# Performance work log

Hardware: AMD Instinct MI355X
Metric: run time of the kernel (lower is better)

The kernel has to match this reference:

```python
import jax, jax.numpy as jnp
import numpy as np

COMMITMENT_COST = 0.25

def setup_inputs() -> dict:
    key = jax.random.key(0)
    k1, k2 = jax.random.split(key)
    B, d_latent = 8192, 512
    ncb, K, d_sub = 2, 8192, 256
    z = jax.random.normal(k1, (B, d_latent), dtype=jnp.float32)
    # original inits uniform(-1/K, 1/K)
    embedding = jax.random.uniform(k2, (ncb, K, d_sub), dtype=jnp.float32,
                                   minval=-1.0 / K, maxval=1.0 / K)
    return {"z": z, "embedding": embedding}


def reference(z, embedding):
    B, d_latent = z.shape
    ncb, K, d_sub = embedding.shape
    z_split = z.reshape(B, ncb, d_sub)

    # squared euclidean distances [B, ncb, K] via ||z||^2 - 2 z.e + ||e||^2
    z_sq = jnp.sum(z_split * z_split, axis=-1)          # [B, ncb]
    e_sq = jnp.sum(embedding * embedding, axis=-1)      # [ncb, K]
    cross = jnp.einsum('bnd,nkd->bnk', z_split, embedding)  # [B, ncb, K]
    distances = z_sq[:, :, None] - 2.0 * cross + e_sq[None, :, :]

    indices = jnp.argmin(distances, axis=-1)            # [B, ncb] int

    # gather quantized vectors: q[b, n] = embedding[n, indices[b, n]]
    cb_ids = jnp.arange(ncb)[None, :]                   # [1, ncb]
    z_q = embedding[cb_ids, indices]                    # [B, ncb, d_sub]

    commitment_loss = COMMITMENT_COST * jnp.mean(
        (z_split - jax.lax.stop_gradient(z_q)) ** 2)
    codebook_loss = jnp.array(0.0, dtype=z.dtype)       # use_ema=True, eval mode

    # straight-through estimator
    z_q_st = z_split + jax.lax.stop_gradient(z_q - z_split)
    quantized = z_q_st.reshape(B, d_latent)

    # perplexity: mean one-hot usage over batch, averaged across codebooks
    counts = jnp.zeros((ncb, K), dtype=z.dtype).at[cb_ids, indices].add(1.0)
    avg_probs = jnp.mean(counts / B, axis=0)            # [K]
    perplexity = jnp.exp(-jnp.sum(avg_probs * jnp.log(avg_probs + 1e-10)))

    return quantized, indices, commitment_loss, codebook_loss, perplexity
```

## Files before the change

### kernel.cpp

```cpp
#include <hip/hip_runtime.h>
#include <hip/hip_fp16.h>


#define KCODES 8192
#define DSUB   256
#define BROWS  8192
#define NROWS  16384
#define NWIN   512

#define QUANT_N  (BROWS * 512)
#define IDX_OFF  QUANT_N
#define LOSS_OFF (QUANT_N + NROWS)

#define WS_ESQ     0
#define WS_ZSQ     65536
#define WS_ZSCL    131072
#define WS_WINNER  262144
#define WS_ZQ      1048576
#define WS_EQ8     5242880
#define WS_TM      9437184

#define EPS 2.5e-4f
#define SE_INV (8192.0f * 127.0f)
#define SE (1.0f / SE_INV)


typedef __attribute__((ext_vector_type(4)))  int int4v;
typedef __attribute__((ext_vector_type(16))) int int16v;

__device__ inline void gl2lds16(const void* g, void* l) {
  __builtin_amdgcn_global_load_lds(
      (const __attribute__((address_space(1))) void*)g,
      (__attribute__((address_space(3))) void*)l, 16, 0, 0);
}

__device__ inline int imax2(int a, int b) { return a > b ? a : b; }

__global__ __launch_bounds__(256)
void prep_kernel(const float* __restrict__ z, const float* __restrict__ e,
                 float* __restrict__ e_sq, float* __restrict__ z_sq,
                 float* __restrict__ z_scl,
                 char* __restrict__ zq, char* __restrict__ eq8,
                 unsigned long long* __restrict__ winner) {
  __shared__ char xfer[4][8192];
  int t = blockIdx.x * 256 + threadIdx.x;
  if (t < 16384) winner[t] = ~0ull;

  const int w = threadIdx.x >> 6, lane = threadIdx.x & 63;
  const int gi = blockIdx.x * 4 + w;
  const int q = lane >> 4, c = lane & 15;
  const bool is_e = gi < 512;
  const int n = (gi >> 8) & 1, g = gi & 255;

  char* dst = (is_e ? eq8 : zq) + (size_t)n * 2097152 + (size_t)g * 8192;

  #pragma unroll 2
  for (int i = 0; i < 8; ++i) {
    const int rr = i * 4 + q;
    const float* src;
    if (is_e) src = e + ((size_t)(n * KCODES + g * 32 + rr)) * DSUB;
    else      src = z + ((size_t)(g * 32 + rr)) * 512 + n * 256;

    float4 f[4];
    float ssq = 0.f, mx = 0.f;
    #pragma unroll
    for (int j = 0; j < 4; ++j) {
      f[j] = *(const float4*)(src + 4 * c + 64 * j);
      ssq += f[j].x * f[j].x + f[j].y * f[j].y + f[j].z * f[j].z + f[j].w * f[j].w;
      mx = fmaxf(mx, fmaxf(fmaxf(fabsf(f[j].x), fabsf(f[j].y)),
                           fmaxf(fabsf(f[j].z), fabsf(f[j].w))));
    }
    #pragma unroll
    for (int off = 8; off; off >>= 1) {
      ssq += __shfl_xor(ssq, off, 16);
      mx = fmaxf(mx, __shfl_xor(mx, off, 16));
    }
    float inv, s = 0.f;
    if (is_e) {
      inv = SE_INV;
    } else {
      s = fmaxf(mx, 1e-20f) * (1.0f / 127.0f);
      inv = 1.0f / s;
    }
    if (c == 0) {
      if (is_e) {
        e_sq[n * KCODES + g * 32 + rr] = ssq;
      } else {
        z_sq[(g * 32 + rr) * 2 + n] = ssq;
        z_scl[n * KCODES + g * 32 + rr] = s;
      }
    }
    #pragma unroll
    for (int j = 0; j < 4; ++j) {
      unsigned acc = 0;
      int q0 = __float2int_rn(fminf(fmaxf(f[j].x * inv, -127.f), 127.f));
      int q1 = __float2int_rn(fminf(fmaxf(f[j].y * inv, -127.f), 127.f));
      int q2 = __float2int_rn(fminf(fmaxf(f[j].z * inv, -127.f), 127.f));
      int q3 = __float2int_rn(fminf(fmaxf(f[j].w * inv, -127.f), 127.f));
      acc = ((unsigned)(q0 & 255)) | ((unsigned)(q1 & 255) << 8)
          | ((unsigned)(q2 & 255) << 16) | ((unsigned)(q3 & 255) << 24);
      const int k = 4 * c + 64 * j;
      const int off = (k >> 5) * 1024 + ((k >> 4) & 1) * 512 + rr * 16 + (k & 15);
      *(unsigned*)&xfer[w][off] = acc;
    }
  }
  __syncthreads();
  #pragma unroll
  for (int it = 0; it < 8; ++it)
    *(uint4*)(dst + it * 1024 + lane * 16) = *(const uint4*)&xfer[w][it * 1024 + lane * 16];
}

__global__ __launch_bounds__(256, 2)
void passA_kernel(const char* __restrict__ zq, const char* __restrict__ eq8,
                  const float* __restrict__ z_scl,
                  unsigned* __restrict__ tm32, int rowoff) {
  __shared__ char Bs[2][8192];

  const int n    = blockIdx.z;
  const int tid  = threadIdx.x;
  const int w    = tid >> 6, lane = tid & 63;
  const int l5   = lane >> 5, c32 = lane & 31;
  const int cb   = blockIdx.x * 512 + w * 128;
  const int rg   = rowoff + blockIdx.y * 256;

  const char* en = eq8 + (size_t)n * 2097152;
  const char* zn = zq + (size_t)n * 2097152;
  const float* zscl = z_scl + n * KCODES;
  unsigned* tmn = tm32 + (size_t)n * (4096 * NWIN);

  const int lo8 = l5 * 512 + c32 * 16;

  int4v areg[8][4];
  #pragma unroll
  for (int k0 = 0; k0 < 8; ++k0)
    #pragma unroll
    for (int mi = 0; mi < 4; ++mi)
      areg[k0][mi] = *(const int4v*)(en + (size_t)((cb >> 5) + mi) * 8192
                                     + k0 * 1024 + lo8);

  const char* zg = zn + (size_t)(rg >> 5) * 8192;
  #pragma unroll
  for (int j = 0; j < 2; ++j)
    gl2lds16(zg + w * 2048 + j * 1024 + lane * 16, &Bs[0][w * 2048 + j * 1024]);

  for (int nt = 0; nt < 8; ++nt) {
    __syncthreads();
    if (nt < 7) {
      const char* zs = zg + (nt + 1) * 8192;
      char* ld = &Bs[(nt + 1) & 1][0];
      #pragma unroll
      for (int j = 0; j < 2; ++j)
        gl2lds16(zs + w * 2048 + j * 1024 + lane * 16, ld + w * 2048 + j * 1024);
    }
    const char* bsrc = &Bs[nt & 1][0];
    const int rowbase = rg + nt * 32;

    const float sv = 2.0f * SE * zscl[rowbase + c32];
    const int thr_i = (int)fminf(EPS / sv, 1.0e9f) + 1;

    int16v acc[4];
    #pragma unroll
    for (int mi = 0; mi < 4; ++mi)
      #pragma unroll
      for (int i = 0; i < 16; ++i) acc[mi][i] = 0;

    #pragma unroll
    for (int k0 = 0; k0 < 8; ++k0) {
      int4v b0 = *(const int4v*)&bsrc[k0 * 1024 + lo8];
      __builtin_amdgcn_s_setprio(1);
      acc[0] = __builtin_amdgcn_mfma_i32_32x32x32_i8(areg[k0][0], b0, acc[0], 0, 0, 0);
      acc[1] = __builtin_amdgcn_mfma_i32_32x32x32_i8(areg[k0][1], b0, acc[1], 0, 0, 0);
      acc[2] = __builtin_amdgcn_mfma_i32_32x32x32_i8(areg[k0][2], b0, acc[2], 0, 0, 0);
      acc[3] = __builtin_amdgcn_mfma_i32_32x32x32_i8(areg[k0][3], b0, acc[3], 0, 0, 0);
      __builtin_amdgcn_s_setprio(0);
    }

    unsigned wd[8];
    #pragma unroll
    for (int mi = 0; mi < 4; ++mi) {
      int mx0 = imax2(imax2(imax2(acc[mi][0], acc[mi][1]), imax2(acc[mi][2], acc[mi][3])),
                      imax2(imax2(acc[mi][4], acc[mi][5]), imax2(acc[mi][6], acc[mi][7])));
      int mx1 = imax2(imax2(imax2(acc[mi][8], acc[mi][9]), imax2(acc[mi][10], acc[mi][11])),
                      imax2(imax2(acc[mi][12], acc[mi][13]), imax2(acc[mi][14], acc[mi][15])));
      mx0 = imax2(mx0, __shfl_xor(mx0, 32, 64));
      mx1 = imax2(mx1, __shfl_xor(mx1, 32, 64));
      unsigned a0 = 0, b0m = 0;
      #pragma unroll
      for (int r = 0; r < 8; ++r) {
        const int bp = (r & 3) + 8 * (r >> 2);
        a0  |= (unsigned)(mx0 - acc[mi][r] <= thr_i) << bp;
        b0m |= (unsigned)(mx1 - acc[mi][r + 8] <= thr_i) << bp;
      }
      a0 <<= 4 * l5;
      b0m <<= 4 * l5;
      a0  |= (unsigned)__shfl_xor((int)a0, 32, 64);
      b0m |= (unsigned)__shfl_xor((int)b0m, 32, 64);
      const float m0f = -sv * (float)mx0;
      const float m1f = -sv * (float)mx1;
      wd[mi * 2]     = (unsigned)__half_as_ushort(__float2half(m0f)) | (a0 << 16);
      wd[mi * 2 + 1] = (unsigned)__half_as_ushort(__float2half(m1f)) | (b0m << 16);
    }
    if (l5 == 0) {
      int zr = rowbase + c32;
      unsigned* dst = &tmn[(size_t)(zr - rowoff) * NWIN + (cb >> 4)];
      uint4 o0; o0.x = wd[0]; o0.y = wd[1]; o0.z = wd[2]; o0.w = wd[3];
      uint4 o1; o1.x = wd[4]; o1.y = wd[5]; o1.z = wd[6]; o1.w = wd[7];
      *(uint4*)dst = o0;
      *(uint4*)(dst + 4) = o1;
    }
  }
}

__global__ __launch_bounds__(256)
void passB12_kernel(const unsigned* __restrict__ tm32, const float* __restrict__ z,
                    const float* __restrict__ emb, const float* __restrict__ e_sq,
                    const float* __restrict__ z_sq,
                    unsigned long long* __restrict__ winner, int rzoff) {
  __shared__ unsigned buf[4][128];

  const int w = threadIdx.x >> 6, lane = threadIdx.x & 63;
  const int gw = blockIdx.x * 4 + w;
  const int r0 = rzoff + gw * 2;
  const int boff = rzoff >> 1;

  unsigned cnt = 0;
  #pragma unroll
  for (int i = 0; i < 2; ++i) {
    const int rz = r0 + i;
    const int nn = rz & 1, b = rz >> 1;
    const unsigned* p = tm32 + ((size_t)nn * 4096 + (b - boff)) * NWIN + lane * 8;
    uint4 ta = *(const uint4*)p;
    uint4 tb = *(const uint4*)(p + 4);
    unsigned wv[8] = {ta.x, ta.y, ta.z, ta.w, tb.x, tb.y, tb.z, tb.w};
    float v[8];
    #pragma unroll
    for (int j = 0; j < 8; ++j)
      v[j] = __half2float(__ushort_as_half((unsigned short)(wv[j] & 0xFFFFu)));
    float mv = v[0];
    #pragma unroll
    for (int j = 1; j < 8; ++j) mv = fminf(mv, v[j]);
    #pragma unroll
    for (int off = 32; off; off >>= 1) mv = fminf(mv, __shfl_xor(mv, off, 64));
    const float thr = mv + EPS;
    #pragma unroll
    for (int j = 0; j < 8; ++j) {
      unsigned long long mb = __ballot(v[j] <= thr);
      while (mb) {
        int src = __ffsll(mb) - 1;
        mb &= mb - 1;
        unsigned word = (unsigned)__shfl((int)wv[j], src, 64);
        unsigned msk = word >> 16;
        int win = src * 8 + j;
        while (msk) {
          int bit = __ffs(msk) - 1;
          msk &= msk - 1;
          if (cnt < 128) {
            if (lane == 0) buf[w][cnt] = ((unsigned)rz << 13) | (unsigned)(win * 16 + bit);
            ++cnt;
          }
        }
      }
    }
  }
  __syncthreads();

  const int g = lane >> 4, l16 = lane & 15;
  for (unsigned idx = (unsigned)g; idx < cnt; idx += 4) {
    unsigned e = buf[w][idx];
    int rz = (int)(e >> 13), code = (int)(e & 8191u), nn = rz & 1;
    const float4* ep = (const float4*)(emb + ((size_t)nn * KCODES + code) * DSUB);
    const float4* zp = (const float4*)(z + (size_t)rz * DSUB);
    float s = 0.f;
    #pragma unroll
    for (int u = 0; u < 4; ++u) {
      float4 ev = ep[l16 + 16 * u];
      float4 zv = zp[l16 + 16 * u];
      s += ev.x * zv.x; s += ev.y * zv.y; s += ev.z * zv.z; s += ev.w * zv.w;
    }
    s += __shfl_xor(s, 1, 64);
    s += __shfl_xor(s, 2, 64);
    s += __shfl_xor(s, 4, 64);
    s += __shfl_xor(s, 8, 64);
    if (l16 == 0) {
      float bd = (z_sq[rz] - 2.0f * s) + e_sq[nn * KCODES + code];
      atomicMin(&winner[rz],
                ((unsigned long long)__float_as_uint(bd) << 32) | (unsigned)code);
    }
  }
}

__global__ __launch_bounds__(256)
void passB3F_kernel(const float* __restrict__ emb,
                    const unsigned long long* __restrict__ winner,
                    float* __restrict__ out) {
  __shared__ int hist[KCODES];
  __shared__ float red[256];

  if (blockIdx.x < 1024) {
    const int w = threadIdx.x >> 6, lane = threadIdx.x & 63;
    const int gw = blockIdx.x * 4 + w;
    const int r0 = gw * 4;

    unsigned long long wv[4];
    #pragma unroll
    for (int i = 0; i < 4; ++i) wv[i] = winner[r0 + i];

    float4 ev[4];
    #pragma unroll
    for (int i = 0; i < 4; ++i) {
      int bk = (int)(unsigned)wv[i];
      ev[i] = ((const float4*)(emb + ((size_t)((r0 + i) & 1) * KCODES + bk) * DSUB))[lane];
    }
    #pragma unroll
    for (int i = 0; i < 4; ++i)
      ((float4*)(out + (size_t)(r0 + i) * DSUB))[lane] = ev[i];

    if (lane < 4) {
      out[IDX_OFF + r0 + lane] = (float)(unsigned)(unsigned)wv[lane];
    }
    return;
  }

  for (int k = threadIdx.x; k < KCODES; k += 256) hist[k] = 0;
  __syncthreads();
  float ls = 0.f;
  #pragma unroll 4
  for (int i = 0; i < 64; ++i) {
    unsigned long long wv = winner[i * 256 + threadIdx.x];
    atomicAdd(&hist[(unsigned)wv & 8191u], 1);
    ls += __uint_as_float((unsigned)(wv >> 32));
  }
  __syncthreads();
  float h = 0.f;
  for (int k = threadIdx.x; k < KCODES; k += 256) {
    float p = (float)hist[k] * (1.0f / 16384.0f);
    h -= p * logf(p + 1e-10f);
  }
  red[threadIdx.x] = h;
  __syncthreads();
  for (int s = 128; s; s >>= 1) {
    if (threadIdx.x < s) red[threadIdx.x] += red[threadIdx.x + s];
    __syncthreads();
  }
  float hsum = red[0];
  __syncthreads();
  red[threadIdx.x] = ls;
  __syncthreads();
  for (int s = 128; s; s >>= 1) {
    if (threadIdx.x < s) red[threadIdx.x] += red[threadIdx.x + s];
    __syncthreads();
  }
  if (threadIdx.x == 0) {
    out[LOSS_OFF + 0] = 0.25f * red[0] * (1.0f / (float)QUANT_N);
    out[LOSS_OFF + 1] = 0.0f;
    out[LOSS_OFF + 2] = expf(hsum);
  }
}

extern "C" void kernel_launch(void* const* d_in, const int* in_sizes, int n_in,
                              void* d_out, int out_size, void* d_ws, size_t ws_size,
                              hipStream_t stream) {
  const float* z   = (const float*)d_in[0];
  const float* emb = (const float*)d_in[1];
  float* out = (float*)d_out;
  char*  ws  = (char*)d_ws;

  float* e_sq   = (float*)(ws + WS_ESQ);
  float* z_sq   = (float*)(ws + WS_ZSQ);
  float* z_scl  = (float*)(ws + WS_ZSCL);
  unsigned long long* winner = (unsigned long long*)(ws + WS_WINNER);
  char* zq  = ws + WS_ZQ;
  char* eq8 = ws + WS_EQ8;
  unsigned* tm32 = (unsigned*)(ws + WS_TM);

  prep_kernel<<<256, 256, 0, stream>>>(z, emb, e_sq, z_sq, z_scl, zq, eq8, winner);
  for (int c = 0; c < 2; ++c) {
    dim3 gA(16, 16, 2);
    passA_kernel<<<gA, 256, 0, stream>>>(zq, eq8, z_scl, tm32, c * 4096);
    passB12_kernel<<<1024, 256, 0, stream>>>(tm32, z, emb, e_sq, z_sq, winner, c * 8192);
  }
  passB3F_kernel<<<1025, 256, 0, stream>>>(emb, winner, out);
}
```

Baseline: 171.9 us.

## Coarsen candidate windows to 32 codes and process all rows in one pass

Each pass-A summary word now covers a 32-code window, with one max and a 16-bit mask in which each bit marks a pair of codes, instead of one word per 16-code window. This halves the intermediate buffer, which now fits the whole batch, so the two-chunk loop is replaced by single launches of pass A and pass B12. The cost is coarser candidate filtering: every set bit forces two codes into exact fp32 rescoring, so pass B12 can gather more candidates, and the per-warp candidate cap of 126 is reached sooner.

New measurement: 157.8 us. 1.09x faster.

```diff
diff --git a/kernel.cpp b/kernel.cpp
--- a/kernel.cpp
+++ b/kernel.cpp
@@ -6,7 +6,7 @@
 #define DSUB   256
 #define BROWS  8192
 #define NROWS  16384
-#define NWIN   512
+#define NWIN2  256
 
 #define QUANT_N  (BROWS * 512)
 #define IDX_OFF  QUANT_N
@@ -113,7 +113,7 @@
 __global__ __launch_bounds__(256, 2)
 void passA_kernel(const char* __restrict__ zq, const char* __restrict__ eq8,
                   const float* __restrict__ z_scl,
-                  unsigned* __restrict__ tm32, int rowoff) {
+                  unsigned* __restrict__ tm32) {
   __shared__ char Bs[2][8192];
 
   const int n    = blockIdx.z;
@@ -121,12 +121,12 @@
   const int w    = tid >> 6, lane = tid & 63;
   const int l5   = lane >> 5, c32 = lane & 31;
   const int cb   = blockIdx.x * 512 + w * 128;
-  const int rg   = rowoff + blockIdx.y * 256;
+  const int rg   = blockIdx.y * 256;
 
   const char* en = eq8 + (size_t)n * 2097152;
   const char* zn = zq + (size_t)n * 2097152;
   const float* zscl = z_scl + n * KCODES;
-  unsigned* tmn = tm32 + (size_t)n * (4096 * NWIN);
+  unsigned* tmn = tm32 + (size_t)n * (BROWS * NWIN2);
 
   const int lo8 = l5 * 512 + c32 * 16;
 
@@ -175,38 +175,31 @@
       __builtin_amdgcn_s_setprio(0);
     }
 
-    unsigned wd[8];
+    unsigned wd[4];
     #pragma unroll
     for (int mi = 0; mi < 4; ++mi) {
-      int mx0 = imax2(imax2(imax2(acc[mi][0], acc[mi][1]), imax2(acc[mi][2], acc[mi][3])),
-                      imax2(imax2(acc[mi][4], acc[mi][5]), imax2(acc[mi][6], acc[mi][7])));
+      int mx = imax2(imax2(imax2(acc[mi][0], acc[mi][1]), imax2(acc[mi][2], acc[mi][3])),
+                     imax2(imax2(acc[mi][4], acc[mi][5]), imax2(acc[mi][6], acc[mi][7])));
       int mx1 = imax2(imax2(imax2(acc[mi][8], acc[mi][9]), imax2(acc[mi][10], acc[mi][11])),
                       imax2(imax2(acc[mi][12], acc[mi][13]), imax2(acc[mi][14], acc[mi][15])));
-      mx0 = imax2(mx0, __shfl_xor(mx0, 32, 64));
-      mx1 = imax2(mx1, __shfl_xor(mx1, 32, 64));
-      unsigned a0 = 0, b0m = 0;
+      mx = imax2(mx, mx1);
+      mx = imax2(mx, __shfl_xor(mx, 32, 64));
+      unsigned m = 0;
       #pragma unroll
-      for (int r = 0; r < 8; ++r) {
-        const int bp = (r & 3) + 8 * (r >> 2);
-        a0  |= (unsigned)(mx0 - acc[mi][r] <= thr_i) << bp;
-        b0m |= (unsigned)(mx1 - acc[mi][r + 8] <= thr_i) << bp;
+      for (int r = 0; r < 16; r += 2) {
+        const int bp = ((r & 3) >> 1) + 4 * (r >> 2);
+        unsigned bit = (unsigned)((mx - acc[mi][r] <= thr_i) |
+                                  (mx - acc[mi][r + 1] <= thr_i));
+        m |= bit << bp;
       }
-      a0 <<= 4 * l5;
-      b0m <<= 4 * l5;
-      a0  |= (unsigned)__shfl_xor((int)a0, 32, 64);
-      b0m |= (unsigned)__shfl_xor((int)b0m, 32, 64);
-      const float m0f = -sv * (float)mx0;
-      const float m1f = -sv * (float)mx1;
-      wd[mi * 2]     = (unsigned)__half_as_ushort(__float2half(m0f)) | (a0 << 16);
-      wd[mi * 2 + 1] = (unsigned)__half_as_ushort(__float2half(m1f)) | (b0m << 16);
+      m <<= 2 * l5;
+      m |= (unsigned)__shfl_xor((int)m, 32, 64);
+      wd[mi] = (unsigned)__half_as_ushort(__float2half(-sv * (float)mx)) | (m << 16);
     }
     if (l5 == 0) {
       int zr = rowbase + c32;
-      unsigned* dst = &tmn[(size_t)(zr - rowoff) * NWIN + (cb >> 4)];
-      uint4 o0; o0.x = wd[0]; o0.y = wd[1]; o0.z = wd[2]; o0.w = wd[3];
-      uint4 o1; o1.x = wd[4]; o1.y = wd[5]; o1.z = wd[6]; o1.w = wd[7];
-      *(uint4*)dst = o0;
-      *(uint4*)(dst + 4) = o1;
+      uint4 o; o.x = wd[0]; o.y = wd[1]; o.z = wd[2]; o.w = wd[3];
+      *(uint4*)&tmn[(size_t)zr * NWIN2 + (cb >> 5)] = o;
     }
   }
 }
@@ -215,48 +208,46 @@
 void passB12_kernel(const unsigned* __restrict__ tm32, const float* __restrict__ z,
                     const float* __restrict__ emb, const float* __restrict__ e_sq,
                     const float* __restrict__ z_sq,
-                    unsigned long long* __restrict__ winner, int rzoff) {
+                    unsigned long long* __restrict__ winner) {
   __shared__ unsigned buf[4][128];
 
   const int w = threadIdx.x >> 6, lane = threadIdx.x & 63;
   const int gw = blockIdx.x * 4 + w;
-  const int r0 = rzoff + gw * 2;
-  const int boff = rzoff >> 1;
+  const int r0 = gw * 2;
 
   unsigned cnt = 0;
   #pragma unroll
   for (int i = 0; i < 2; ++i) {
     const int rz = r0 + i;
     const int nn = rz & 1, b = rz >> 1;
-    const unsigned* p = tm32 + ((size_t)nn * 4096 + (b - boff)) * NWIN + lane * 8;
-    uint4 ta = *(const uint4*)p;
-    uint4 tb = *(const uint4*)(p + 4);
-    unsigned wv[8] = {ta.x, ta.y, ta.z, ta.w, tb.x, tb.y, tb.z, tb.w};
-    float v[8];
-    #pragma unroll
-    for (int j = 0; j < 8; ++j)
+    uint4 ta = *(const uint4*)(tm32 + ((size_t)nn * BROWS + b) * NWIN2 + lane * 4);
+    unsigned wv[4] = {ta.x, ta.y, ta.z, ta.w};
+    float v[4];
+    #pragma unroll
+    for (int j = 0; j < 4; ++j)
       v[j] = __half2float(__ushort_as_half((unsigned short)(wv[j] & 0xFFFFu)));
-    float mv = v[0];
-    #pragma unroll
-    for (int j = 1; j < 8; ++j) mv = fminf(mv, v[j]);
+    float mv = fminf(fminf(v[0], v[1]), fminf(v[2], v[3]));
     #pragma unroll
     for (int off = 32; off; off >>= 1) mv = fminf(mv, __shfl_xor(mv, off, 64));
     const float thr = mv + EPS;
     #pragma unroll
-    for (int j = 0; j < 8; ++j) {
+    for (int j = 0; j < 4; ++j) {
       unsigned long long mb = __ballot(v[j] <= thr);
       while (mb) {
         int src = __ffsll(mb) - 1;
         mb &= mb - 1;
         unsigned word = (unsigned)__shfl((int)wv[j], src, 64);
         unsigned msk = word >> 16;
-        int win = src * 8 + j;
+        int win = src * 4 + j;
         while (msk) {
           int bit = __ffs(msk) - 1;
           msk &= msk - 1;
-          if (cnt < 128) {
-            if (lane == 0) buf[w][cnt] = ((unsigned)rz << 13) | (unsigned)(win * 16 + bit);
-            ++cnt;
+          if (cnt < 126) {
+            if (lane == 0) {
+              buf[w][cnt]     = ((unsigned)rz << 13) | (unsigned)(win * 32 + bit * 2);
+              buf[w][cnt + 1] = ((unsigned)rz << 13) | (unsigned)(win * 32 + bit * 2 + 1);
+            }
+            cnt += 2;
           }
         }
       }
@@ -374,10 +365,8 @@
   unsigned* tm32 = (unsigned*)(ws + WS_TM);
 
   prep_kernel<<<256, 256, 0, stream>>>(z, emb, e_sq, z_sq, z_scl, zq, eq8, winner);
-  for (int c = 0; c < 2; ++c) {
-    dim3 gA(16, 16, 2);
-    passA_kernel<<<gA, 256, 0, stream>>>(zq, eq8, z_scl, tm32, c * 4096);
-    passB12_kernel<<<1024, 256, 0, stream>>>(tm32, z, emb, e_sq, z_sq, winner, c * 8192);
-  }
+  dim3 gA(16, 32, 2);
+  passA_kernel<<<gA, 256, 0, stream>>>(zq, eq8, z_scl, tm32);
+  passB12_kernel<<<2048, 256, 0, stream>>>(tm32, z, emb, e_sq, z_sq, winner);
   passB3F_kernel<<<1025, 256, 0, stream>>>(emb, winner, out);
 }
```
